# Optimization experiments

Measured on AMD Instinct MI355X. Metric: run time of the kernel, lower is better.

The kernel has to match this reference:

```python
import math
import jax, jax.numpy as jnp
import numpy as np

V, D, H, L, F, T, B = 32000, 1024, 16, 4, 4096, 1024, 2
HD = D // H
EPS = 1e-5


def make_pe(max_len, d):
    pos = np.arange(max_len)[:, None].astype(np.float32)
    div = np.exp(np.arange(0, d, 2).astype(np.float32) * (-math.log(10000.0) / d))
    pe = np.zeros((max_len, d), dtype=np.float32)
    pe[:, 0::2] = np.sin(pos * div)
    pe[:, 1::2] = np.cos(pos * div)
    return jnp.asarray(pe)


def setup_inputs() -> dict:
    key = jax.random.key(0)
    ks = jax.random.split(key, 12)
    s = 0.02
    inp = {
        'tokens': jax.random.randint(ks[0], (B, T), 0, V, dtype=jnp.int32),
        'mask': jnp.tril(jnp.ones((T, T), dtype=jnp.int32)),
        'emb': jax.random.normal(ks[1], (V, D), jnp.float32) * s,
        'pe': make_pe(T, D),
        'ln1_g': jnp.ones((L, D)), 'ln1_b': jnp.zeros((L, D)),
        'Wqkv': jax.random.normal(ks[2], (L, D, 3 * D), jnp.float32) * s,
        'bqkv': jnp.zeros((L, 3 * D)),
        'Wproj': jax.random.normal(ks[3], (L, D, D), jnp.float32) * s,
        'bproj': jnp.zeros((L, D)),
        'ln2_g': jnp.ones((L, D)), 'ln2_b': jnp.zeros((L, D)),
        'W1': jax.random.normal(ks[4], (L, D, F), jnp.float32) * s,
        'b1': jnp.zeros((L, F)),
        'W2': jax.random.normal(ks[5], (L, F, D), jnp.float32) * s,
        'b2': jnp.zeros((L, D)),
        'lnf_g': jnp.ones((D,)), 'lnf_b': jnp.zeros((D,)),
        'out_b': jnp.zeros((V,)),
    }
    return inp


def layer_norm(x, g, b):
    m = jnp.mean(x, axis=-1, keepdims=True)
    v = jnp.mean((x - m) ** 2, axis=-1, keepdims=True)
    return (x - m) / jnp.sqrt(v + EPS) * g + b


def attention(x, mask, Wqkv, bqkv, Wproj, bproj):
    b, t, c = x.shape
    qkv = (x @ Wqkv + bqkv).reshape(b, t, 3, H, HD)
    q, k, v = jnp.moveaxis(qkv, 2, 0)  # each [B,T,H,HD]
    q = q.transpose(0, 2, 1, 3)  # [B,H,T,HD]
    k = k.transpose(0, 2, 1, 3)
    v = v.transpose(0, 2, 1, 3)
    scores = jnp.einsum('bhqd,bhkd->bhqk', q, k) / math.sqrt(HD)
    scores = jnp.where(mask[None, None] == 0, -1e9, scores)
    attn = jax.nn.softmax(scores, axis=-1)
    out = jnp.einsum('bhqk,bhkd->bhqd', attn, v)
    out = out.transpose(0, 2, 1, 3).reshape(b, t, c)
    return out @ Wproj + bproj, attn


def reference(tokens, mask, emb, pe, ln1_g, ln1_b, Wqkv, bqkv, Wproj, bproj,
              ln2_g, ln2_b, W1, b1, W2, b2, lnf_g, lnf_b, out_b):
    x = emb[tokens] + pe[:tokens.shape[1]]
    attn = None
    for i in range(L):
        a, attn = attention(layer_norm(x, ln1_g[i], ln1_b[i]), mask,
                            Wqkv[i], bqkv[i], Wproj[i], bproj[i])
        x = x + a
        h = layer_norm(x, ln2_g[i], ln2_b[i])
        h = jax.nn.gelu(h @ W1[i] + b1[i], approximate=False) @ W2[i] + b2[i]
        x = x + h
    x = layer_norm(x, lnf_g, lnf_b)
    logits = x @ emb.T + out_b  # weight tying
    return logits, attn
```

## Files before the change

kernel.cpp:

```cpp
#include <hip/hip_runtime.h>
#include <cstdint>

#define DEV static __device__ __forceinline__

typedef unsigned short u16;
typedef __bf16 bf16x8 __attribute__((ext_vector_type(8)));
typedef float f32x4 __attribute__((ext_vector_type(4)));
typedef unsigned short u16x4 __attribute__((ext_vector_type(4)));

constexpr int V = 32000, D = 1024, H = 16, L = 4, F = 4096, T = 1024, B = 2;
constexpr int HD = 64;

DEV u16 f2bf(float f) {
    union { float f; uint32_t i; } c; c.f = f;
    uint32_t x = c.i;
    return (u16)((x + 0x7fffu + ((x >> 16) & 1u)) >> 16);
}
DEV bf16x8 ld8(const u16* p) { return *reinterpret_cast<const bf16x8*>(p); }

DEV void gl16(const void* g, void* l) {
    __builtin_amdgcn_global_load_lds((const __attribute__((address_space(1))) void*)g,
                                     (__attribute__((address_space(3))) void*)l, 16, 0, 0);
}

__global__ __launch_bounds__(256) void k_embln(const int* __restrict__ tok,
        const float* __restrict__ emb, const float* __restrict__ pe,
        const float* __restrict__ g, const float* __restrict__ b,
        float* __restrict__ x, u16* __restrict__ out) {
    int row = blockIdx.x, tid = threadIdx.x;
    int t = row & (T - 1);
    int vv = tok[row];
    f32x4 v = ((const f32x4*)(emb + (size_t)vv * D))[tid] + ((const f32x4*)(pe + (size_t)t * D))[tid];
    ((f32x4*)(x + (size_t)row * D))[tid] = v;
    float s = v[0] + v[1] + v[2] + v[3];
    float s2 = v[0]*v[0] + v[1]*v[1] + v[2]*v[2] + v[3]*v[3];
#pragma unroll
    for (int m = 1; m < 64; m <<= 1) { s += __shfl_xor(s, m); s2 += __shfl_xor(s2, m); }
    __shared__ float ps[4], ps2[4];
    int wave = tid >> 6;
    if ((tid & 63) == 0) { ps[wave] = s; ps2[wave] = s2; }
    __syncthreads();
    s = ps[0] + ps[1] + ps[2] + ps[3];
    s2 = ps2[0] + ps2[1] + ps2[2] + ps2[3];
    float mean = s * (1.f / D);
    float var = s2 * (1.f / D) - mean * mean;
    float r = rsqrtf(var + 1e-5f);
    f32x4 gg = ((const f32x4*)g)[tid];
    f32x4 bb = ((const f32x4*)b)[tid];
    u16x4 o;
#pragma unroll
    for (int j = 0; j < 4; j++) o[j] = f2bf((v[j] - mean) * r * gg[j] + bb[j]);
    ((u16x4*)(out + (size_t)row * D))[tid] = o;
}

template <int S>
__global__ __launch_bounds__(256) void k_redln(const float* __restrict__ pp,
        const float* __restrict__ bias, float* __restrict__ x,
        const float* __restrict__ g, const float* __restrict__ b,
        u16* __restrict__ out) {
    int row = blockIdx.x, tid = threadIdx.x;
    f32x4 v = ((const f32x4*)(x + (size_t)row * D))[tid];
#pragma unroll
    for (int s = 0; s < S; s++)
        v += ((const f32x4*)(pp + ((size_t)s * (B * T) + row) * D))[tid];
    v += ((const f32x4*)bias)[tid];
    ((f32x4*)(x + (size_t)row * D))[tid] = v;
    float s = v[0] + v[1] + v[2] + v[3];
    float s2 = v[0]*v[0] + v[1]*v[1] + v[2]*v[2] + v[3]*v[3];
#pragma unroll
    for (int m = 1; m < 64; m <<= 1) { s += __shfl_xor(s, m); s2 += __shfl_xor(s2, m); }
    __shared__ float ps[4], ps2[4];
    int wave = tid >> 6;
    if ((tid & 63) == 0) { ps[wave] = s; ps2[wave] = s2; }
    __syncthreads();
    s = ps[0] + ps[1] + ps[2] + ps[3];
    s2 = ps2[0] + ps2[1] + ps2[2] + ps2[3];
    float mean = s * (1.f / D);
    float var = s2 * (1.f / D) - mean * mean;
    float r = rsqrtf(var + 1e-5f);
    f32x4 gg = ((const f32x4*)g)[tid];
    f32x4 bb = ((const f32x4*)b)[tid];
    u16x4 o;
#pragma unroll
    for (int j = 0; j < 4; j++) o[j] = f2bf((v[j] - mean) * r * gg[j] + bb[j]);
    ((u16x4*)(out + (size_t)row * D))[tid] = o;
}

__global__ __launch_bounds__(256) void k_cast(const float* __restrict__ src,
        u16* __restrict__ dst) {
    int i = (blockIdx.x * 256 + threadIdx.x) * 4;
    f32x4 v = *(const f32x4*)(src + i);
    u16x4 o;
#pragma unroll
    for (int j = 0; j < 4; j++) o[j] = f2bf(v[j]);
    *(u16x4*)(dst + i) = o;
}

__global__ __launch_bounds__(256) void k_castT4(const float* __restrict__ Wqkv,
        const float* __restrict__ Wproj, const float* __restrict__ W1,
        const float* __restrict__ W2, u16* __restrict__ wt) {
    int bid = blockIdx.x;
    const float* src; u16* dst; int Rr, Cc, t;
    if (bid < 3072)      { src = Wqkv;  dst = wt;                   Rr = D; Cc = 3 * D; t = bid; }
    else if (bid < 4096) { src = Wproj; dst = wt + 3 * D * D;       Rr = D; Cc = D;     t = bid - 3072; }
    else if (bid < 8192) { src = W1;    dst = wt + 4 * D * D;       Rr = D; Cc = F;     t = bid - 4096; }
    else                 { src = W2;    dst = wt + 4 * D * D + D * F; Rr = F; Cc = D;   t = bid - 8192; }
    int ntx = Cc >> 5;
    int c0 = (t % ntx) * 32, r0 = (t / ntx) * 32;
    __shared__ u16 tl[32][33];
    int x = threadIdx.x & 31, y = threadIdx.x >> 5;
#pragma unroll
    for (int i = 0; i < 4; i++)
        tl[y + i * 8][x] = f2bf(src[(size_t)(r0 + y + i * 8) * Cc + c0 + x]);
    __syncthreads();
#pragma unroll
    for (int i = 0; i < 4; i++)
        dst[(size_t)(c0 + y + i * 8) * Rr + r0 + x] = tl[x][y + i * 8];
}

DEV bf16x8 ldf(const u16* half, int row, int lhi) {
    int lb = row * 64 + lhi * 16;
    lb ^= ((lb >> 9) & 1) << 5;
    return *(const bf16x8*)((const char*)half + lb);
}
DEV void stg(const u16* gb, int ld, int kc, u16* dstBase, int wave, int lane) {
#pragma unroll
    for (int i = 0; i < 2; i++) {
        int p = (wave * 2 + i) * 64 + lane;
        int l = p ^ (((p >> 5) & 1) << 1);
        gl16(gb + (size_t)(l >> 2) * ld + kc + (l & 3) * 8, dstBase + (wave * 2 + i) * 512);
    }
}
#define SB_BAR() do { __builtin_amdgcn_sched_barrier(0); __builtin_amdgcn_s_barrier(); } while (0)

template <int EPI, bool VT>
__global__ __launch_bounds__(256, 2) void k_gemm4(
        const u16* __restrict__ A, int lda,
        const u16* __restrict__ Bt, int ldb,
        const float* __restrict__ bias,
        void* __restrict__ Cv, int ldc, int K, u16* __restrict__ vT) {
    __shared__ u16 lds[2][4][128 * 32];
    int gm = gridDim.x, nwg = gm * gridDim.y;
    int orig = blockIdx.y * gm + blockIdx.x;
    int xcd = orig & 7, idx = orig >> 3;
    int q = nwg >> 3, rr = nwg & 7;
    int wg = (xcd < rr ? xcd * (q + 1) : rr * (q + 1) + (xcd - rr) * q) + idx;
    int m0 = (wg % gm) * 128, n0 = (wg / gm) * 128;
    int koff = (EPI == 4) ? blockIdx.z * K : 0;
    int tid = threadIdx.x, wave = tid >> 6, lane = tid & 63;
    int llo = lane & 15, lhi = lane >> 4;
    int wm = wave >> 1, wn = wave & 1;
    const u16* Ab = A + (size_t)m0 * lda;
    const u16* Bb = Bt + (size_t)n0 * ldb;
    int nk = K >> 6;
    f32x4 acc[4][4] = {};
    stg(Ab, lda, koff + 0,   &lds[0][0][0], wave, lane);
    stg(Bb, ldb, koff + 0,   &lds[0][1][0], wave, lane);
    stg(Ab, lda, koff + 32,  &lds[0][2][0], wave, lane);
    stg(Bb, ldb, koff + 32,  &lds[0][3][0], wave, lane);
    stg(Ab, lda, koff + 64,  &lds[1][0][0], wave, lane);
    stg(Bb, ldb, koff + 64,  &lds[1][1][0], wave, lane);
    stg(Ab, lda, koff + 96,  &lds[1][2][0], wave, lane);
    asm volatile("s_waitcnt vmcnt(10)");
    SB_BAR();
    for (int t = 0; t < nk; ++t) {
        const int bf = t & 1;
        bf16x8 af[4], b0, b1;
#pragma unroll
        for (int mi = 0; mi < 4; mi++) af[mi] = ldf(&lds[bf][0][0], wm * 64 + mi * 16 + llo, lhi);
        b0 = ldf(&lds[bf][1][0], wn * 64 + llo, lhi);
        b1 = ldf(&lds[bf][1][0], wn * 64 + 16 + llo, lhi);
        if (t + 1 < nk) stg(Bb, ldb, koff + (t + 1) * 64 + 32, &lds[bf ^ 1][3][0], wave, lane);
        __builtin_amdgcn_s_setprio(1);
#pragma unroll
        for (int mi = 0; mi < 4; mi++) {
            acc[mi][0] = __builtin_amdgcn_mfma_f32_16x16x32_bf16(af[mi], b0, acc[mi][0], 0, 0, 0);
            acc[mi][1] = __builtin_amdgcn_mfma_f32_16x16x32_bf16(af[mi], b1, acc[mi][1], 0, 0, 0);
        }
        __builtin_amdgcn_s_setprio(0);
        SB_BAR();
        b0 = ldf(&lds[bf][1][0], wn * 64 + 32 + llo, lhi);
        b1 = ldf(&lds[bf][1][0], wn * 64 + 48 + llo, lhi);
        if (t + 2 < nk) stg(Ab, lda, koff + (t + 2) * 64, &lds[bf][0][0], wave, lane);
        __builtin_amdgcn_s_setprio(1);
#pragma unroll
        for (int mi = 0; mi < 4; mi++) {
            acc[mi][2] = __builtin_amdgcn_mfma_f32_16x16x32_bf16(af[mi], b0, acc[mi][2], 0, 0, 0);
            acc[mi][3] = __builtin_amdgcn_mfma_f32_16x16x32_bf16(af[mi], b1, acc[mi][3], 0, 0, 0);
        }
        __builtin_amdgcn_s_setprio(0);
        if (t + 2 < nk)      { asm volatile("s_waitcnt vmcnt(10)"); }
        else if (t + 1 < nk) { asm volatile("s_waitcnt vmcnt(8)"); }
        else                 { asm volatile("s_waitcnt vmcnt(0)"); }
        SB_BAR();
#pragma unroll
        for (int mi = 0; mi < 4; mi++) af[mi] = ldf(&lds[bf][2][0], wm * 64 + mi * 16 + llo, lhi);
        b0 = ldf(&lds[bf][3][0], wn * 64 + llo, lhi);
        b1 = ldf(&lds[bf][3][0], wn * 64 + 16 + llo, lhi);
        if (t + 2 < nk) stg(Bb, ldb, koff + (t + 2) * 64, &lds[bf][1][0], wave, lane);
        __builtin_amdgcn_s_setprio(1);
#pragma unroll
        for (int mi = 0; mi < 4; mi++) {
            acc[mi][0] = __builtin_amdgcn_mfma_f32_16x16x32_bf16(af[mi], b0, acc[mi][0], 0, 0, 0);
            acc[mi][1] = __builtin_amdgcn_mfma_f32_16x16x32_bf16(af[mi], b1, acc[mi][1], 0, 0, 0);
        }
        __builtin_amdgcn_s_setprio(0);
        SB_BAR();
        b0 = ldf(&lds[bf][3][0], wn * 64 + 32 + llo, lhi);
        b1 = ldf(&lds[bf][3][0], wn * 64 + 48 + llo, lhi);
        if (t + 2 < nk) stg(Ab, lda, koff + (t + 2) * 64 + 32, &lds[bf][2][0], wave, lane);
        __builtin_amdgcn_s_setprio(1);
#pragma unroll
        for (int mi = 0; mi < 4; mi++) {
            acc[mi][2] = __builtin_amdgcn_mfma_f32_16x16x32_bf16(af[mi], b0, acc[mi][2], 0, 0, 0);
            acc[mi][3] = __builtin_amdgcn_mfma_f32_16x16x32_bf16(af[mi], b1, acc[mi][3], 0, 0, 0);
        }
        __builtin_amdgcn_s_setprio(0);
        if (t + 1 < nk) {
            if (t + 2 < nk) { asm volatile("s_waitcnt vmcnt(10)"); }
            else            { asm volatile("s_waitcnt vmcnt(4)"); }
        }
        SB_BAR();
    }
#pragma unroll
    for (int ni = 0; ni < 4; ni++) {
        int col = n0 + wn * 64 + ni * 16 + llo;
        float bb = 0.f;
        if (EPI != 4) bb = bias[col];
#pragma unroll
        for (int mi = 0; mi < 4; mi++) {
            int row0 = m0 + wm * 64 + mi * 16 + lhi * 4;
            if (VT && col >= 2 * D) {
                int dv = col - 2 * D;
                int b_ = row0 >> 10, t_ = row0 & (T - 1);
                u16x4 pk;
#pragma unroll
                for (int r = 0; r < 4; r++) pk[r] = f2bf(acc[mi][ni][r] + bb);
                *(u16x4*)(vT + ((size_t)(b_ * 16 + (dv >> 6)) * HD + (dv & 63)) * T + t_) = pk;
            } else {
#pragma unroll
                for (int r = 0; r < 4; r++) {
                    int row = row0 + r;
                    float o = acc[mi][ni][r] + bb;
                    if (EPI == 1) o = 0.5f * o * (1.f + erff(o * 0.70710678118f));
                    if (EPI == 4) {
                        ((float*)Cv)[((size_t)blockIdx.z * (B * T) + row) * ldc + col] = o;
                    } else {
                        ((u16*)Cv)[(size_t)row * ldc + col] = f2bf(o);
                    }
                }
            }
        }
    }
}

__global__ __launch_bounds__(512, 2) void k_gemm8(
        const u16* __restrict__ A, int lda,
        const u16* __restrict__ Bt, int ldb,
        const float* __restrict__ bias,
        float* __restrict__ C, int ldc, int K) {
    __shared__ u16 lds[2][4][256 * 32];
    int gm = gridDim.x, nwg = gm * gridDim.y;
    int orig = blockIdx.y * gm + blockIdx.x;
    int xcd = orig & 7, idx = orig >> 3;
    int q = nwg >> 3, rr = nwg & 7;
    int wg = (xcd < rr ? xcd * (q + 1) : rr * (q + 1) + (xcd - rr) * q) + idx;
    int m0 = (wg % gm) * 256, n0 = (wg / gm) * 256;
    int tid = threadIdx.x, wave = tid >> 6, lane = tid & 63;
    int llo = lane & 15, lhi = lane >> 4;
    int wm = wave >> 2, wn = wave & 3;
    const u16* Ab = A + (size_t)m0 * lda;
    const u16* Bb = Bt + (size_t)n0 * ldb;
    int nk = K >> 6;
    f32x4 acc[8][4] = {};
    stg(Ab, lda, 0,   &lds[0][0][0], wave, lane);
    stg(Bb, ldb, 0,   &lds[0][1][0], wave, lane);
    stg(Ab, lda, 32,  &lds[0][2][0], wave, lane);
    stg(Bb, ldb, 32,  &lds[0][3][0], wave, lane);
    stg(Ab, lda, 64,  &lds[1][0][0], wave, lane);
    stg(Bb, ldb, 64,  &lds[1][1][0], wave, lane);
    stg(Ab, lda, 96,  &lds[1][2][0], wave, lane);
    asm volatile("s_waitcnt vmcnt(10)");
    SB_BAR();
    for (int t = 0; t < nk; ++t) {
        const int bf = t & 1;
        bf16x8 af[8], b0, b1;
#pragma unroll
        for (int mi = 0; mi < 8; mi++) af[mi] = ldf(&lds[bf][0][0], wm * 128 + mi * 16 + llo, lhi);
        b0 = ldf(&lds[bf][1][0], wn * 64 + llo, lhi);
        b1 = ldf(&lds[bf][1][0], wn * 64 + 16 + llo, lhi);
        if (t + 1 < nk) stg(Bb, ldb, (t + 1) * 64 + 32, &lds[bf ^ 1][3][0], wave, lane);
        __builtin_amdgcn_s_setprio(1);
#pragma unroll
        for (int mi = 0; mi < 8; mi++) {
            acc[mi][0] = __builtin_amdgcn_mfma_f32_16x16x32_bf16(af[mi], b0, acc[mi][0], 0, 0, 0);
            acc[mi][1] = __builtin_amdgcn_mfma_f32_16x16x32_bf16(af[mi], b1, acc[mi][1], 0, 0, 0);
        }
        __builtin_amdgcn_s_setprio(0);
        SB_BAR();
        b0 = ldf(&lds[bf][1][0], wn * 64 + 32 + llo, lhi);
        b1 = ldf(&lds[bf][1][0], wn * 64 + 48 + llo, lhi);
        if (t + 2 < nk) stg(Ab, lda, (t + 2) * 64, &lds[bf][0][0], wave, lane);
        __builtin_amdgcn_s_setprio(1);
#pragma unroll
        for (int mi = 0; mi < 8; mi++) {
            acc[mi][2] = __builtin_amdgcn_mfma_f32_16x16x32_bf16(af[mi], b0, acc[mi][2], 0, 0, 0);
            acc[mi][3] = __builtin_amdgcn_mfma_f32_16x16x32_bf16(af[mi], b1, acc[mi][3], 0, 0, 0);
        }
        __builtin_amdgcn_s_setprio(0);
        if (t + 2 < nk)      { asm volatile("s_waitcnt vmcnt(10)"); }
        else if (t + 1 < nk) { asm volatile("s_waitcnt vmcnt(8)"); }
        else                 { asm volatile("s_waitcnt vmcnt(0)"); }
        SB_BAR();
#pragma unroll
        for (int mi = 0; mi < 8; mi++) af[mi] = ldf(&lds[bf][2][0], wm * 128 + mi * 16 + llo, lhi);
        b0 = ldf(&lds[bf][3][0], wn * 64 + llo, lhi);
        b1 = ldf(&lds[bf][3][0], wn * 64 + 16 + llo, lhi);
        if (t + 2 < nk) stg(Bb, ldb, (t + 2) * 64, &lds[bf][1][0], wave, lane);
        __builtin_amdgcn_s_setprio(1);
#pragma unroll
        for (int mi = 0; mi < 8; mi++) {
            acc[mi][0] = __builtin_amdgcn_mfma_f32_16x16x32_bf16(af[mi], b0, acc[mi][0], 0, 0, 0);
            acc[mi][1] = __builtin_amdgcn_mfma_f32_16x16x32_bf16(af[mi], b1, acc[mi][1], 0, 0, 0);
        }
        __builtin_amdgcn_s_setprio(0);
        SB_BAR();
        b0 = ldf(&lds[bf][3][0], wn * 64 + 32 + llo, lhi);
        b1 = ldf(&lds[bf][3][0], wn * 64 + 48 + llo, lhi);
        if (t + 2 < nk) stg(Ab, lda, (t + 2) * 64 + 32, &lds[bf][2][0], wave, lane);
        __builtin_amdgcn_s_setprio(1);
#pragma unroll
        for (int mi = 0; mi < 8; mi++) {
            acc[mi][2] = __builtin_amdgcn_mfma_f32_16x16x32_bf16(af[mi], b0, acc[mi][2], 0, 0, 0);
            acc[mi][3] = __builtin_amdgcn_mfma_f32_16x16x32_bf16(af[mi], b1, acc[mi][3], 0, 0, 0);
        }
        __builtin_amdgcn_s_setprio(0);
        if (t + 1 < nk) {
            if (t + 2 < nk) { asm volatile("s_waitcnt vmcnt(10)"); }
            else            { asm volatile("s_waitcnt vmcnt(4)"); }
        }
        SB_BAR();
    }
#pragma unroll
    for (int ni = 0; ni < 4; ni++) {
        int col = n0 + wn * 64 + ni * 16 + llo;
        float bb = bias[col];
#pragma unroll
        for (int mi = 0; mi < 8; mi++) {
            int row0 = m0 + wm * 128 + mi * 16 + lhi * 4;
#pragma unroll
            for (int r = 0; r < 4; r++)
                C[(size_t)(row0 + r) * ldc + col] = acc[mi][ni][r] + bb;
        }
    }
}

template <int PW>
__global__ __launch_bounds__(256) void k_fattn(const u16* __restrict__ qkv,
        const u16* __restrict__ vT, u16* __restrict__ out, float* __restrict__ attnF) {
    __shared__ u16 plds[4][16 * 40];
    int bh = blockIdx.y; int b = bh >> 4, h = bh & 15;
    int tid = threadIdx.x, wave = tid >> 6, lane = tid & 63;
    int llo = lane & 15, lhi = lane >> 4;
    int i0 = blockIdx.x * 64 + wave * 16;
    const u16* qb = qkv + (size_t)b * T * (3 * D) + h * HD;
    const u16* kb = qb + D;
    const u16* vt = vT + (size_t)bh * HD * T;
    bf16x8 q0 = ld8(qb + (size_t)(i0 + llo) * (3 * D) + lhi * 8);
    bf16x8 q1 = ld8(qb + (size_t)(i0 + llo) * (3 * D) + 32 + lhi * 8);
    int qrow = i0 + llo;
    float m = -3e38f, s = 0.f;
    f32x4 oacc[4] = {};
    u16* pw = &plds[wave][0];
    for (int k0 = 0; k0 < i0 + 16; k0 += 32) {
        f32x4 sc0 = {}, sc1 = {};
        {
            bf16x8 kf0 = ld8(kb + (size_t)(k0 + llo) * (3 * D) + lhi * 8);
            bf16x8 kf1 = ld8(kb + (size_t)(k0 + llo) * (3 * D) + 32 + lhi * 8);
            sc0 = __builtin_amdgcn_mfma_f32_16x16x32_bf16(kf0, q0, sc0, 0, 0, 0);
            sc0 = __builtin_amdgcn_mfma_f32_16x16x32_bf16(kf1, q1, sc0, 0, 0, 0);
        }
        if (k0 + 16 < i0 + 16) {
            bf16x8 kf0 = ld8(kb + (size_t)(k0 + 16 + llo) * (3 * D) + lhi * 8);
            bf16x8 kf1 = ld8(kb + (size_t)(k0 + 16 + llo) * (3 * D) + 32 + lhi * 8);
            sc1 = __builtin_amdgcn_mfma_f32_16x16x32_bf16(kf0, q0, sc1, 0, 0, 0);
            sc1 = __builtin_amdgcn_mfma_f32_16x16x32_bf16(kf1, q1, sc1, 0, 0, 0);
        }
        float vv[8]; float mx = m;
#pragma unroll
        for (int hf = 0; hf < 2; hf++)
#pragma unroll
            for (int r = 0; r < 4; r++) {
                int k = k0 + hf * 16 + lhi * 4 + r;
                float x = (hf ? sc1[r] : sc0[r]) * 0.125f;
                float v = (k <= qrow) ? x : -3e38f;
                vv[hf * 4 + r] = v;
                mx = fmaxf(mx, v);
            }
        mx = fmaxf(mx, __shfl_xor(mx, 16));
        mx = fmaxf(mx, __shfl_xor(mx, 32));
        float p[8]; float ps = 0.f;
#pragma unroll
        for (int j = 0; j < 8; j++) { p[j] = __expf(vv[j] - mx); ps += p[j]; }
        ps += __shfl_xor(ps, 16);
        ps += __shfl_xor(ps, 32);
        float scale = __expf(m - mx);
        s = s * scale + ps;
        m = mx;
        float sr[4];
#pragma unroll
        for (int r = 0; r < 4; r++) sr[r] = __shfl(scale, lhi * 4 + r);
#pragma unroll
        for (int n = 0; n < 4; n++)
#pragma unroll
            for (int r = 0; r < 4; r++) oacc[n][r] *= sr[r];
#pragma unroll
        for (int hf = 0; hf < 2; hf++) {
            u16x4 pk;
#pragma unroll
            for (int r = 0; r < 4; r++) pk[r] = f2bf(p[hf * 4 + r]);
            *(u16x4*)(pw + llo * 40 + hf * 16 + lhi * 4) = pk;
        }
        bf16x8 pa = ld8(pw + llo * 40 + lhi * 8);
#pragma unroll
        for (int n = 0; n < 4; n++) {
            bf16x8 vb = ld8(vt + (size_t)(n * 16 + llo) * T + k0 + lhi * 8);
            oacc[n] = __builtin_amdgcn_mfma_f32_16x16x32_bf16(pa, vb, oacc[n], 0, 0, 0);
        }
    }
    float inv = 1.f / s;
    float ir[4];
#pragma unroll
    for (int r = 0; r < 4; r++) ir[r] = __shfl(inv, lhi * 4 + r);
#pragma unroll
    for (int n = 0; n < 4; n++)
#pragma unroll
        for (int r = 0; r < 4; r++) {
            int i = i0 + lhi * 4 + r, c = n * 16 + llo;
            out[(size_t)(b * T + i) * D + h * HD + c] = f2bf(oacc[n][r] * ir[r]);
        }
    if (PW) {
        float* ar = attnF + ((size_t)bh * T + qrow) * T;
        for (int j0 = 0; j0 < T; j0 += 16) {
            f32x4 pv = {};
            if (j0 <= qrow) {
                if (j0 < i0 + 16) {
                    bf16x8 kf0 = ld8(kb + (size_t)(j0 + llo) * (3 * D) + lhi * 8);
                    bf16x8 kf1 = ld8(kb + (size_t)(j0 + llo) * (3 * D) + 32 + lhi * 8);
                    f32x4 sc = {};
                    sc = __builtin_amdgcn_mfma_f32_16x16x32_bf16(kf0, q0, sc, 0, 0, 0);
                    sc = __builtin_amdgcn_mfma_f32_16x16x32_bf16(kf1, q1, sc, 0, 0, 0);
#pragma unroll
                    for (int r = 0; r < 4; r++) {
                        int j = j0 + lhi * 4 + r;
                        pv[r] = (j <= qrow) ? __expf(sc[r] * 0.125f - m) * inv : 0.f;
                    }
                }
            }
            *(f32x4*)(ar + j0 + lhi * 4) = pv;
        }
    }
}

extern "C" void kernel_launch(void* const* d_in, const int* in_sizes, int n_in,
                              void* d_out, int out_size, void* d_ws, size_t ws_size,
                              hipStream_t stream) {
    const int*   tok   = (const int*)d_in[0];
    const float* emb   = (const float*)d_in[2];
    const float* pe    = (const float*)d_in[3];
    const float* ln1g  = (const float*)d_in[4];
    const float* ln1b  = (const float*)d_in[5];
    const float* Wqkv  = (const float*)d_in[6];
    const float* bqkv  = (const float*)d_in[7];
    const float* Wproj = (const float*)d_in[8];
    const float* bproj = (const float*)d_in[9];
    const float* ln2g  = (const float*)d_in[10];
    const float* ln2b  = (const float*)d_in[11];
    const float* W1    = (const float*)d_in[12];
    const float* b1    = (const float*)d_in[13];
    const float* W2    = (const float*)d_in[14];
    const float* b2    = (const float*)d_in[15];
    const float* lnfg  = (const float*)d_in[16];
    const float* lnfb  = (const float*)d_in[17];
    const float* outb  = (const float*)d_in[18];

    float* logits  = (float*)d_out;
    float* attnF   = logits + (size_t)B * T * V;

    char* w = (char*)d_ws;
    float* x    = (float*)w;  w += (size_t)B * T * D * 4;
    u16* lnout  = (u16*)w;    w += (size_t)B * T * D * 2;
    u16* qkv    = (u16*)w;    w += (size_t)B * T * 3 * D * 2;
    u16* vT     = (u16*)w;    w += (size_t)B * H * HD * T * 2;
    u16* aout   = (u16*)w;    w += (size_t)B * T * D * 2;
    char* tail = w;
    u16* hmid   = (u16*)w;    w += (size_t)B * T * F * 2;
    u16* WTL    = (u16*)w;    w += (size_t)(5 * D * D + 2 * D * F) * 2;
    float* pp   = (float*)w;  w += (size_t)4 * B * T * D * 4;
    u16* embB   = (u16*)tail;

    dim3 blk(256);
    k_embln<<<dim3(B * T), blk, 0, stream>>>(tok, emb, pe, ln1g, ln1b, x, lnout);

    for (int l = 0; l < L; l++) {
        k_castT4<<<dim3(12288), blk, 0, stream>>>(
            Wqkv + (size_t)l * D * 3 * D, Wproj + (size_t)l * D * D,
            W1 + (size_t)l * D * F, W2 + (size_t)l * F * D, WTL);
        k_gemm4<0, true><<<dim3(B * T / 128, 3 * D / 128), blk, 0, stream>>>(
            lnout, D, WTL, D, bqkv + l * 3 * D, qkv, 3 * D, D, vT);
        if (l == L - 1)
            k_fattn<1><<<dim3(T / 64, B * H), blk, 0, stream>>>(qkv, vT, aout, attnF);
        else
            k_fattn<0><<<dim3(T / 64, B * H), blk, 0, stream>>>(qkv, vT, aout, attnF);
        k_gemm4<4, false><<<dim3(B * T / 128, D / 128, 2), blk, 0, stream>>>(
            aout, D, WTL + (size_t)3 * D * D, D, nullptr, pp, D, D / 2, nullptr);
        k_redln<2><<<dim3(B * T), blk, 0, stream>>>(pp, bproj + l * D, x,
            ln2g + l * D, ln2b + l * D, lnout);
        k_gemm4<1, false><<<dim3(B * T / 128, F / 128), blk, 0, stream>>>(
            lnout, D, WTL + (size_t)4 * D * D, D, b1 + l * F, hmid, F, D, nullptr);
        k_gemm4<4, false><<<dim3(B * T / 128, D / 128, 4), blk, 0, stream>>>(
            hmid, F, WTL + (size_t)4 * D * D + D * F, F, nullptr, pp, D, F / 4, nullptr);
        const float* ng = (l == L - 1) ? lnfg : ln1g + (l + 1) * D;
        const float* nb = (l == L - 1) ? lnfb : ln1b + (l + 1) * D;
        k_redln<4><<<dim3(B * T), blk, 0, stream>>>(pp, b2 + l * D, x, ng, nb, lnout);
    }
    k_cast<<<dim3(V * D / 1024), blk, 0, stream>>>(emb, embB);
    k_gemm8<<<dim3(B * T / 256, V / 256), dim3(512), 0, stream>>>(
        lnout, D, embB, D, outb, logits, V, D);
}
```

Before: 996.2 us.

## Fuse per-layer weight cast/transpose into LayerNorm kernels and split Wproj K four ways

The separate per-layer weight transpose-cast kernel is removed. Its work is appended as extra blocks to the embedding-LN kernel and to the end-of-layer residual-LN kernel, with each block now handling a 32x128 strip, which saves a launch per layer and lets the cast overlap with the row-wise LN work. The Wproj GEMM split-K goes from 2 to 4 slices so it launches more blocks, at the cost of reducing one extra partial buffer in the following LN. Because the next layer's weights are written during the previous layer's final LN, the ordering relies on WTL no longer being read by then.

```diff
diff --git a/kernel.cpp b/kernel.cpp
--- a/kernel.cpp
+++ b/kernel.cpp
@@ -23,11 +23,45 @@
                                      (__attribute__((address_space(3))) void*)l, 16, 0, 0);
 }
 
-__global__ __launch_bounds__(256) void k_embln(const int* __restrict__ tok,
+DEV void castT4_dev(int t, int x, int y, u16 (*tl)[33],
+        const float* __restrict__ Wqkv, const float* __restrict__ Wproj,
+        const float* __restrict__ W1, const float* __restrict__ W2,
+        u16* __restrict__ wt) {
+    const float* src; u16* dst; int Rr, Cc;
+    if (t < 768)       { src = Wqkv;  dst = wt;                       Rr = D; Cc = 3 * D; }
+    else if (t < 1024) { src = Wproj; dst = wt + 3 * D * D;           Rr = D; Cc = D; t -= 768; }
+    else if (t < 2048) { src = W1;    dst = wt + 4 * D * D;           Rr = D; Cc = F; t -= 1024; }
+    else               { src = W2;    dst = wt + 4 * D * D + D * F;   Rr = F; Cc = D; t -= 2048; }
+    int colStrips = Cc >> 7;
+    int r0 = (t / colStrips) * 32;
+    int c0 = (t % colStrips) * 128;
+    for (int i = 0; i < 4; i++) {
+        int cc = c0 + i * 32;
+        __syncthreads();
+#pragma unroll
+        for (int j = 0; j < 4; j++)
+            tl[y + j * 8][x] = f2bf(src[(size_t)(r0 + y + j * 8) * Cc + cc + x]);
+        __syncthreads();
+#pragma unroll
+        for (int j = 0; j < 4; j++)
+            dst[(size_t)(cc + y + j * 8) * Rr + r0 + x] = tl[x][y + j * 8];
+    }
+}
+
+__global__ __launch_bounds__(256) void k_emblnT(const int* __restrict__ tok,
         const float* __restrict__ emb, const float* __restrict__ pe,
         const float* __restrict__ g, const float* __restrict__ b,
-        float* __restrict__ x, u16* __restrict__ out) {
+        float* __restrict__ x, u16* __restrict__ out,
+        const float* __restrict__ Wqkv, const float* __restrict__ Wproj,
+        const float* __restrict__ W1, const float* __restrict__ W2,
+        u16* __restrict__ wt) {
+    __shared__ u16 tl[32][33];
+    __shared__ float ps[4], ps2[4];
     int row = blockIdx.x, tid = threadIdx.x;
+    if (row >= B * T) {
+        castT4_dev(row - B * T, tid & 31, tid >> 5, tl, Wqkv, Wproj, W1, W2, wt);
+        return;
+    }
     int t = row & (T - 1);
     int vv = tok[row];
     f32x4 v = ((const f32x4*)(emb + (size_t)vv * D))[tid] + ((const f32x4*)(pe + (size_t)t * D))[tid];
@@ -36,7 +70,6 @@
     float s2 = v[0]*v[0] + v[1]*v[1] + v[2]*v[2] + v[3]*v[3];
 #pragma unroll
     for (int m = 1; m < 64; m <<= 1) { s += __shfl_xor(s, m); s2 += __shfl_xor(s2, m); }
-    __shared__ float ps[4], ps2[4];
     int wave = tid >> 6;
     if ((tid & 63) == 0) { ps[wave] = s; ps2[wave] = s2; }
     __syncthreads();
@@ -53,12 +86,21 @@
     ((u16x4*)(out + (size_t)row * D))[tid] = o;
 }
 
-template <int S>
-__global__ __launch_bounds__(256) void k_redln(const float* __restrict__ pp,
+template <int S, bool DOCAST>
+__global__ __launch_bounds__(256) void k_redlnT(const float* __restrict__ pp,
         const float* __restrict__ bias, float* __restrict__ x,
         const float* __restrict__ g, const float* __restrict__ b,
-        u16* __restrict__ out) {
+        u16* __restrict__ out,
+        const float* __restrict__ Wqkv, const float* __restrict__ Wproj,
+        const float* __restrict__ W1, const float* __restrict__ W2,
+        u16* __restrict__ wt) {
+    __shared__ u16 tl[32][33];
+    __shared__ float ps[4], ps2[4];
     int row = blockIdx.x, tid = threadIdx.x;
+    if (DOCAST && row >= B * T) {
+        castT4_dev(row - B * T, tid & 31, tid >> 5, tl, Wqkv, Wproj, W1, W2, wt);
+        return;
+    }
     f32x4 v = ((const f32x4*)(x + (size_t)row * D))[tid];
 #pragma unroll
     for (int s = 0; s < S; s++)
@@ -69,7 +111,6 @@
     float s2 = v[0]*v[0] + v[1]*v[1] + v[2]*v[2] + v[3]*v[3];
 #pragma unroll
     for (int m = 1; m < 64; m <<= 1) { s += __shfl_xor(s, m); s2 += __shfl_xor(s2, m); }
-    __shared__ float ps[4], ps2[4];
     int wave = tid >> 6;
     if ((tid & 63) == 0) { ps[wave] = s; ps2[wave] = s2; }
     __syncthreads();
@@ -94,28 +135,6 @@
 #pragma unroll
     for (int j = 0; j < 4; j++) o[j] = f2bf(v[j]);
     *(u16x4*)(dst + i) = o;
-}
-
-__global__ __launch_bounds__(256) void k_castT4(const float* __restrict__ Wqkv,
-        const float* __restrict__ Wproj, const float* __restrict__ W1,
-        const float* __restrict__ W2, u16* __restrict__ wt) {
-    int bid = blockIdx.x;
-    const float* src; u16* dst; int Rr, Cc, t;
-    if (bid < 3072)      { src = Wqkv;  dst = wt;                   Rr = D; Cc = 3 * D; t = bid; }
-    else if (bid < 4096) { src = Wproj; dst = wt + 3 * D * D;       Rr = D; Cc = D;     t = bid - 3072; }
-    else if (bid < 8192) { src = W1;    dst = wt + 4 * D * D;       Rr = D; Cc = F;     t = bid - 4096; }
-    else                 { src = W2;    dst = wt + 4 * D * D + D * F; Rr = F; Cc = D;   t = bid - 8192; }
-    int ntx = Cc >> 5;
-    int c0 = (t % ntx) * 32, r0 = (t / ntx) * 32;
-    __shared__ u16 tl[32][33];
-    int x = threadIdx.x & 31, y = threadIdx.x >> 5;
-#pragma unroll
-    for (int i = 0; i < 4; i++)
-        tl[y + i * 8][x] = f2bf(src[(size_t)(r0 + y + i * 8) * Cc + c0 + x]);
-    __syncthreads();
-#pragma unroll
-    for (int i = 0; i < 4; i++)
-        dst[(size_t)(c0 + y + i * 8) * Rr + r0 + x] = tl[x][y + i * 8];
 }
 
 DEV bf16x8 ldf(const u16* half, int row, int lhi) {
@@ -500,29 +519,34 @@
     u16* embB   = (u16*)tail;
 
     dim3 blk(256);
-    k_embln<<<dim3(B * T), blk, 0, stream>>>(tok, emb, pe, ln1g, ln1b, x, lnout);
+    const int CG = 3072;
+    k_emblnT<<<dim3(B * T + CG), blk, 0, stream>>>(tok, emb, pe, ln1g, ln1b, x, lnout,
+        Wqkv, Wproj, W1, W2, WTL);
 
     for (int l = 0; l < L; l++) {
-        k_castT4<<<dim3(12288), blk, 0, stream>>>(
-            Wqkv + (size_t)l * D * 3 * D, Wproj + (size_t)l * D * D,
-            W1 + (size_t)l * D * F, W2 + (size_t)l * F * D, WTL);
         k_gemm4<0, true><<<dim3(B * T / 128, 3 * D / 128), blk, 0, stream>>>(
             lnout, D, WTL, D, bqkv + l * 3 * D, qkv, 3 * D, D, vT);
         if (l == L - 1)
             k_fattn<1><<<dim3(T / 64, B * H), blk, 0, stream>>>(qkv, vT, aout, attnF);
         else
             k_fattn<0><<<dim3(T / 64, B * H), blk, 0, stream>>>(qkv, vT, aout, attnF);
-        k_gemm4<4, false><<<dim3(B * T / 128, D / 128, 2), blk, 0, stream>>>(
-            aout, D, WTL + (size_t)3 * D * D, D, nullptr, pp, D, D / 2, nullptr);
-        k_redln<2><<<dim3(B * T), blk, 0, stream>>>(pp, bproj + l * D, x,
-            ln2g + l * D, ln2b + l * D, lnout);
+        k_gemm4<4, false><<<dim3(B * T / 128, D / 128, 4), blk, 0, stream>>>(
+            aout, D, WTL + (size_t)3 * D * D, D, nullptr, pp, D, D / 4, nullptr);
+        k_redlnT<4, false><<<dim3(B * T), blk, 0, stream>>>(pp, bproj + l * D, x,
+            ln2g + l * D, ln2b + l * D, lnout, nullptr, nullptr, nullptr, nullptr, nullptr);
         k_gemm4<1, false><<<dim3(B * T / 128, F / 128), blk, 0, stream>>>(
             lnout, D, WTL + (size_t)4 * D * D, D, b1 + l * F, hmid, F, D, nullptr);
         k_gemm4<4, false><<<dim3(B * T / 128, D / 128, 4), blk, 0, stream>>>(
             hmid, F, WTL + (size_t)4 * D * D + D * F, F, nullptr, pp, D, F / 4, nullptr);
-        const float* ng = (l == L - 1) ? lnfg : ln1g + (l + 1) * D;
-        const float* nb = (l == L - 1) ? lnfb : ln1b + (l + 1) * D;
-        k_redln<4><<<dim3(B * T), blk, 0, stream>>>(pp, b2 + l * D, x, ng, nb, lnout);
+        if (l < L - 1) {
+            k_redlnT<4, true><<<dim3(B * T + CG), blk, 0, stream>>>(pp, b2 + l * D, x,
+                ln1g + (l + 1) * D, ln1b + (l + 1) * D, lnout,
+                Wqkv + (size_t)(l + 1) * D * 3 * D, Wproj + (size_t)(l + 1) * D * D,
+                W1 + (size_t)(l + 1) * D * F, W2 + (size_t)(l + 1) * F * D, WTL);
+        } else {
+            k_redlnT<4, false><<<dim3(B * T), blk, 0, stream>>>(pp, b2 + l * D, x,
+                lnfg, lnfb, lnout, nullptr, nullptr, nullptr, nullptr, nullptr);
+        }
     }
     k_cast<<<dim3(V * D / 1024), blk, 0, stream>>>(emb, embB);
     k_gemm8<<<dim3(B * T / 256, V / 256), dim3(512), 0, stream>>>(
```

After: 998.4 us. No clear change (+0.2%).
